# Kernel optimization log

Hardware: AMD Instinct MI355X
Metric: run time of the kernel (lower is better)

## Reference

```python
import jax, jax.numpy as jnp
import numpy as np

B, L, H, C, K, S = 32, 512, 336, 321, 8, 8   # batch, seq_len, pred_len, channels, leaders, states
FREQ = H // 2 + 1                            # 169
G = 2 * K + 1                                # filter groups
TEMP = 1.0
EPS = 1e-5


def setup_inputs() -> dict:
    key = jax.random.key(0)
    ks = jax.random.split(key, 12)
    x = jax.random.normal(ks[0], (B, L, C), jnp.float32)
    leader_ids = jax.random.randint(ks[1], (B, C, K), 0, C)
    shift = jax.random.randint(ks[2], (B, C, K), 0, L)
    r = jax.random.normal(ks[3], (B, C, K), jnp.float32)
    # backbone linear: seq_len -> pred_len
    Wb = jax.random.normal(ks[4], (H, L), jnp.float32) * float(1.0 / np.sqrt(L))
    bb = jnp.zeros((H,), jnp.float32)
    # factory classifier: (L + K) features -> state_num logits
    Wc = jax.random.normal(ks[5], (S, L + K), jnp.float32) * float(1.0 / np.sqrt(L + K))
    bc = jnp.zeros((S,), jnp.float32)
    # state prototype filters (complex, stored as re/im): [S, 2K+1, FREQ]
    states_re = jax.random.normal(ks[6], (S, G, FREQ), jnp.float32) * float(1.0 / np.sqrt(S))
    states_im = jax.random.normal(ks[7], (S, G, FREQ), jnp.float32) * float(1.0 / np.sqrt(S))
    # complex mix layer: 3*FREQ -> FREQ
    Wm_re = jax.random.normal(ks[8], (FREQ, 3 * FREQ), jnp.float32) * float(1.0 / np.sqrt(3 * FREQ))
    Wm_im = jax.random.normal(ks[9], (FREQ, 3 * FREQ), jnp.float32) * float(1.0 / np.sqrt(3 * FREQ))
    bm_re = jnp.zeros((FREQ,), jnp.float32)
    bm_im = jnp.zeros((FREQ,), jnp.float32)
    return dict(x=x, r=r, Wb=Wb, bb=bb, Wc=Wc, bc=bc,
                states_re=states_re, states_im=states_im,
                Wm_re=Wm_re, Wm_im=Wm_im, bm_re=bm_re, bm_im=bm_im,
                leader_ids=leader_ids, shift=shift)


def reference(x, r, Wb, bb, Wc, bc, states_re, states_im, Wm_re, Wm_im, bm_re, bm_im, leader_ids, shift):
    xc = jnp.transpose(x, (0, 2, 1))                      # [B,C,L]
    mu = xc.mean(-1, keepdims=True)
    norm = jnp.sqrt(xc.var(-1, keepdims=True) + EPS)
    xn = (xc - mu) / norm                                 # instance_norm
    y_hat = jnp.einsum('bcl,hl->bch', xn, Wb) + bb        # backbone [B,C,H]

    # --- shifted_leader_seq (torch.no_grad) ---
    full = jax.lax.stop_gradient(jnp.concatenate([xn, y_hat], -1))      # [B,C,L+H]
    lead_full = full[jnp.arange(B)[:, None, None], leader_ids]          # [B,C,K,L+H]
    t_idx = (L - shift)[..., None] + jnp.arange(H)                      # [B,C,K,H]
    seq_shifted = jnp.take_along_axis(lead_full, t_idx, axis=-1)        # [B,C,K,H]
    r = jax.lax.stop_gradient(r)

    # softmax leader weights with leading constant-one slot
    ones = jnp.ones((B, C, 1), xn.dtype)
    r_soft = jax.nn.softmax(jnp.concatenate([ones, jnp.abs(r)], -1) / TEMP, axis=-1)  # [B,C,K+1]

    # --- factory: state-mixed complex filters ---
    feat = jnp.concatenate([xn, r_soft[..., 1:]], -1)                   # [B,C,L+K]
    p = jax.nn.softmax(jnp.einsum('bcf,sf->bcs', feat, Wc) + bc, axis=-1)
    states = states_re + 1j * states_im                                 # [S,G,FREQ]
    filters = jnp.einsum('bcs,sgf->bcgf', p, states)                    # [B,C,2K+1,FREQ]

    # --- FFT filter multiply-sum + inverse FFT mix ---
    y_hat_f = jnp.fft.rfft(y_hat)                                       # [B,C,FREQ]
    seq_shifted_f = jnp.fft.rfft(seq_shifted) * filters[:, :, :K]       # [B,C,K,FREQ]
    seq_diff_f = (seq_shifted_f - y_hat_f[:, :, None]) * filters[:, :, K:-1]
    yh_f = y_hat_f * filters[:, :, -1]
    z = jnp.concatenate([seq_shifted_f.sum(2), seq_diff_f.sum(2), yh_f], -1)  # [B,C,3*FREQ]
    Wm = Wm_re + 1j * Wm_im
    mixed = jnp.einsum('bcf,gf->bcg', z, Wm) + (bm_re + 1j * bm_im)     # [B,C,FREQ]
    y_hat = y_hat + jnp.fft.irfft(mixed, n=H)

    y = y_hat * norm + mu
    return jnp.transpose(y, (0, 2, 1))                                  # [B,H,C]
```

## Files before the change

### kernel.cpp

```cpp
#include <hip/hip_runtime.h>
#include <math.h>

#define B_ 32
#define L_ 512
#define H_ 336
#define C_ 321
#define K_ 8
#define S_ 8
#define FREQ_ 169
#define G_ 17
#define LHB_ 848
#define F_FEAT 520
#define EPS_ 1e-5f
#define BCN_ (B_ * C_)
#define DZB_ 7

#ifndef M_PIf
#define M_PIf 3.14159265358979323846f
#endif

typedef __attribute__((ext_vector_type(8))) short short8v;
typedef __attribute__((ext_vector_type(4))) float f32x4;

__device__ __forceinline__ unsigned short f2bf(float x) {
    unsigned u = __builtin_bit_cast(unsigned, x);
    u += 0x7FFFu + ((u >> 16) & 1u);
    return (unsigned short)(u >> 16);
}
__device__ __forceinline__ float bf2f(unsigned short h) {
    return __builtin_bit_cast(float, (unsigned)h << 16);
}

__global__ __launch_bounds__(256) void k_prepA(const float* __restrict__ Wb,
                                               const float* __restrict__ st_re,
                                               const float* __restrict__ st_im,
                                               unsigned short* __restrict__ Tdft,
                                               float* __restrict__ ctb,
                                               float* __restrict__ stb,
                                               unsigned short* __restrict__ Wbsw,
                                               float4* __restrict__ stf4,
                                               float2* __restrict__ stg3) {
    int bid = blockIdx.x, tid = threadIdx.x;
    if (bid < 61) {
        int orig = bid * 4 + (tid >> 6);
        if (orig < 11 * 22) {
            int lane = tid & 63;
            int kc = orig / 22, nt = orig % 22;
            int n = nt * 16 + (lane & 15);
            int kb = kc * 32 + (lane >> 4) * 8;
            int f = n >> 1;
            unsigned short* dst = Tdft + (size_t)orig * 512 + lane * 8;
            for (int i = 0; i < 8; ++i) {
                int k = kb + i;
                float val = 0.f;
                if (k < H_ && n < 2 * FREQ_) {
                    int m = (k * f) % H_;
                    float s, c;
                    sincosf((float)m * (2.0f * M_PIf / (float)H_), &s, &c);
                    val = (n & 1) ? -s : c;
                }
                dst[i] = f2bf(val);
            }
        }
    } else if (bid < 283) {
        int idx = (bid - 61) * 256 + tid;
        if (idx < FREQ_ * H_) {
            int g = idx / H_, h = idx % H_;
            int m = (g * h) % H_;
            float s, c;
            sincosf((float)m * (2.0f * M_PIf / (float)H_), &s, &c);
            float wgt = ((g == 0 || g == FREQ_ - 1) ? 1.0f : 2.0f) * (1.0f / (float)H_);
            ctb[idx] = wgt * c;
            stb[idx] = -wgt * s;
        }
    } else if (bid < 367) {
        int orig = (bid - 283) * 4 + (tid >> 6);
        if (orig < 16 * 21) {
            int lane = tid & 63;
            int kc = orig / 21, nt = orig % 21;
            int n = nt * 16 + (lane & 15);
            int kb = kc * 32 + (lane >> 4) * 8;
            unsigned short* dst = Wbsw + (size_t)orig * 512 + lane * 8;
            for (int i = 0; i < 8; ++i) {
                int k = kb + i;
                dst[i] = f2bf(Wb[(size_t)n * L_ + k]);
            }
        }
    } else {
        int idx = (bid - 367) * 256 + tid;
        if (idx < 64 * FREQ_) {
            int row = idx / FREQ_, f = idx % FREQ_;
            int k = row >> 3, s = row & 7;
            size_t b1 = (size_t)s * (G_ * FREQ_) + (size_t)k * FREQ_ + f;
            size_t b2 = (size_t)s * (G_ * FREQ_) + (size_t)(8 + k) * FREQ_ + f;
            stf4[idx] = make_float4(st_re[b1], st_im[b1], st_re[b2], st_im[b2]);
        }
        if (idx < 8 * FREQ_) {
            int s = idx / FREQ_, f = idx % FREQ_;
            size_t b3 = (size_t)s * (G_ * FREQ_) + (size_t)16 * FREQ_ + f;
            stg3[idx] = make_float2(st_re[b3], st_im[b3]);
        }
    }
}

__global__ __launch_bounds__(256) void k_prepB(const float* __restrict__ Wm_re,
                                               const float* __restrict__ Wm_im,
                                               const float* __restrict__ bm_re,
                                               const float* __restrict__ bm_im,
                                               const float* __restrict__ ctb,
                                               const float* __restrict__ stb,
                                               unsigned short* __restrict__ T,
                                               float* __restrict__ bvec) {
    int bid = blockIdx.x, tid = threadIdx.x;
    if (bid < 672) {
        int t = bid * 256 + tid;
        if (t >= 512 * H_) return;
        int k = t / H_, h = t - k * H_;
        float s1 = 0.f, s2 = 0.f;
        if (k < 3 * FREQ_) {
            #pragma unroll 4
            for (int g = 0; g < FREQ_; ++g) {
                float ct = ctb[g * H_ + h];
                float st = stb[g * H_ + h];
                float wr = Wm_re[(size_t)g * (3 * FREQ_) + k];
                float wi = Wm_im[(size_t)g * (3 * FREQ_) + k];
                s1 += wr * ct + wi * st;
                s2 += wr * st - wi * ct;
            }
        }
        int nt = h >> 4, nr = h & 15;
        {
            int kc = k >> 5, kr = k & 31;
            int lane = ((kr >> 3) << 4) | nr;
            T[((size_t)(kc * 21 + nt)) * 512 + lane * 8 + (k & 7)] = f2bf(s1);
        }
        {
            int kk = k + 512;
            int kc = kk >> 5, kr = kk & 31;
            int lane = ((kr >> 3) << 4) | nr;
            T[((size_t)(kc * 21 + nt)) * 512 + lane * 8 + (kk & 7)] = f2bf(s2);
        }
    } else {
        int h = (bid - 672) * 256 + tid;
        if (h >= H_) return;
        float acc = 0.f;
        for (int g = 0; g < FREQ_; ++g)
            acc += bm_re[g] * ctb[g * H_ + h] + bm_im[g] * stb[g * H_ + h];
        bvec[h] = acc;
    }
}

__global__ __launch_bounds__(256) void k_stats_part(const float* __restrict__ x,
                                                    float2* __restrict__ part) {
    __shared__ float red_s[4][64], red_q[4][64];
    int tid = threadIdx.x, w = tid >> 6, lane = tid & 63;
    int b = blockIdx.y, c0 = blockIdx.x * 64, l0 = blockIdx.z * 64;
    int c = c0 + lane;
    bool valid = (c < C_);
    const float* xb = x + ((size_t)b * L_) * C_;
    float s = 0.f, q = 0.f;
    for (int li = w; li < 64; li += 4) {
        float v = valid ? xb[(size_t)(l0 + li) * C_ + c] : 0.f;
        s += v; q += v * v;
    }
    red_s[w][lane] = s; red_q[w][lane] = q;
    __syncthreads();
    if (w == 0) {
        float S = red_s[0][lane] + red_s[1][lane] + red_s[2][lane] + red_s[3][lane];
        float Q = red_q[0][lane] + red_q[1][lane] + red_q[2][lane] + red_q[3][lane];
        part[(size_t)(((b * 6 + blockIdx.x) * 8) + blockIdx.z) * 64 + lane] = make_float2(S, Q);
    }
}

__global__ __launch_bounds__(256) void k_stats_fin(const float2* __restrict__ part,
                                                   float* __restrict__ muv,
                                                   float* __restrict__ nrm) {
    int t = blockIdx.x * 256 + threadIdx.x;
    int b = t / 384, rem = t % 384;
    int ct = rem / 64, cl = rem % 64;
    int c = ct * 64 + cl;
    if (b >= B_ || c >= C_) return;
    float S = 0.f, Q = 0.f;
    #pragma unroll
    for (int ls = 0; ls < 8; ++ls) {
        float2 p = part[(size_t)(((b * 6 + ct) * 8) + ls) * 64 + cl];
        S += p.x; Q += p.y;
    }
    float mu = S / (float)L_;
    float var = Q / (float)L_ - mu * mu;
    float n = sqrtf(var + EPS_);
    muv[(size_t)b * C_ + c] = mu;
    nrm[(size_t)b * C_ + c] = n;
}

__global__ __launch_bounds__(256) void k_norm(const float* __restrict__ x,
                                              const float* __restrict__ muv,
                                              const float* __restrict__ nrm,
                                              unsigned short* __restrict__ fullbf) {
    __shared__ float tl[64][65];
    int tid = threadIdx.x, w = tid >> 6, lane = tid & 63;
    int b = blockIdx.y, c0 = blockIdx.x * 64, l0 = blockIdx.z * 64;
    int c = c0 + lane;
    bool valid = (c < C_);
    const float* xb = x + ((size_t)b * L_) * C_;
    float mu = valid ? muv[(size_t)b * C_ + c] : 0.f;
    float inv = valid ? (1.0f / nrm[(size_t)b * C_ + c]) : 0.f;
    for (int li = w; li < 64; li += 4) {
        float v = valid ? xb[(size_t)(l0 + li) * C_ + c] : 0.f;
        tl[li][lane] = (v - mu) * inv;
    }
    __syncthreads();
    for (int cr = w; cr < 64; cr += 4) {
        int cc = c0 + cr;
        if (cc < C_ && lane < 32) {
            size_t bc = (size_t)b * C_ + cc;
            unsigned pk = (unsigned)f2bf(tl[2 * lane][cr]) |
                          ((unsigned)f2bf(tl[2 * lane + 1][cr]) << 16);
            ((unsigned*)fullbf)[(bc * LHB_ + l0) / 2 + lane] = pk;
        }
    }
}

__global__ __launch_bounds__(256) void k_yhat(const unsigned short* __restrict__ fullbf_r,
                                              const unsigned short* __restrict__ Wbsw,
                                              const float* __restrict__ bb,
                                              unsigned short* __restrict__ fullbf_w) {
    int bc0 = blockIdx.x * 32;
    int half = blockIdx.y;
    int tid = threadIdx.x, w = tid >> 6, lane = tid & 63;
    const int NTB0[5] = {0, 3, 6, 9, 11};
    const int NTB1[5] = {11, 14, 17, 19, 21};
    int nt0 = half ? NTB1[w] : NTB0[w];
    int ntn = (half ? NTB1[w + 1] : NTB0[w + 1]) - nt0;
    int r15 = lane & 15, kg = lane >> 4;
    f32x4 acc[2][3];
    #pragma unroll
    for (int mf = 0; mf < 2; ++mf)
        #pragma unroll
        for (int j = 0; j < 3; ++j) acc[mf][j] = (f32x4){0.f, 0.f, 0.f, 0.f};
    for (int kc = 0; kc < 16; ++kc) {
        short8v a[2];
        #pragma unroll
        for (int mf = 0; mf < 2; ++mf)
            a[mf] = *(const short8v*)(fullbf_r + ((size_t)(bc0 + mf * 16 + r15) * LHB_ + kc * 32 + kg * 8));
        #pragma unroll
        for (int j = 0; j < 3; ++j) {
            if (j >= ntn) continue;
            short8v bfr = *(const short8v*)(Wbsw + ((size_t)(kc * 21 + nt0 + j) * 512 + lane * 8));
            #pragma unroll
            for (int mf = 0; mf < 2; ++mf)
                acc[mf][j] = __builtin_amdgcn_mfma_f32_16x16x32_bf16(a[mf], bfr, acc[mf][j], 0, 0, 0);
        }
    }
    #pragma unroll
    for (int mf = 0; mf < 2; ++mf)
        #pragma unroll
        for (int j = 0; j < 3; ++j) {
            if (j >= ntn) continue;
            int n_ = (nt0 + j) * 16 + r15;
            #pragma unroll
            for (int reg = 0; reg < 4; ++reg) {
                int bc = bc0 + mf * 16 + kg * 4 + reg;
                fullbf_w[(size_t)bc * LHB_ + L_ + n_] = f2bf(acc[mf][j][reg] + bb[n_]);
            }
        }
}

__global__ __launch_bounds__(256) void k_p2(const unsigned short* __restrict__ fullbf,
                                            const float* __restrict__ r,
                                            const float* __restrict__ Wc,
                                            const float* __restrict__ bcv,
                                            float* __restrict__ p_out) {
    __shared__ float WcS[8 * F_FEAT];
    __shared__ float rsS[16][8];
    __shared__ float bcS[8];
    int tid = threadIdx.x, w = tid >> 6, lane = tid & 63;
    int bc0 = blockIdx.x * 16;
    for (int i = tid; i < 8 * F_FEAT; i += 256) WcS[i] = Wc[i];
    if (tid < 8) bcS[tid] = bcv[tid];
    if (tid < 16) {
        int bc = bc0 + tid;
        const float* rr = r + (size_t)bc * K_;
        float a[8]; float m = 1.0f;
        #pragma unroll
        for (int k = 0; k < 8; ++k) { a[k] = fabsf(rr[k]); m = fmaxf(m, a[k]); }
        float Z = expf(1.0f - m);
        float e[8];
        #pragma unroll
        for (int k = 0; k < 8; ++k) { e[k] = expf(a[k] - m); Z += e[k]; }
        float inv = 1.0f / Z;
        #pragma unroll
        for (int k = 0; k < 8; ++k) rsS[tid][k] = e[k] * inv;
    }
    __syncthreads();

    for (int i = 0; i < 4; ++i) {
        int bcl = w * 4 + i;
        int bc = bc0 + bcl;
        const unsigned* xrow = (const unsigned*)(fullbf + (size_t)bc * LHB_);
        float acc[8] = {0.f, 0.f, 0.f, 0.f, 0.f, 0.f, 0.f, 0.f};
        #pragma unroll
        for (int t = 0; t < 4; ++t) {
            int j = lane + t * 64;
            unsigned v = xrow[j];
            float x0 = bf2f((unsigned short)(v & 0xffff));
            float x1 = bf2f((unsigned short)(v >> 16));
            #pragma unroll
            for (int s = 0; s < 8; ++s)
                acc[s] += x0 * WcS[s * F_FEAT + 2 * j] + x1 * WcS[s * F_FEAT + 2 * j + 1];
        }
        if (lane < 8) {
            float xf = rsS[bcl][lane];
            #pragma unroll
            for (int s = 0; s < 8; ++s) acc[s] += xf * WcS[s * F_FEAT + L_ + lane];
        }
        #pragma unroll
        for (int s = 0; s < 8; ++s) {
            #pragma unroll
            for (int off = 32; off > 0; off >>= 1) acc[s] += __shfl_down(acc[s], off);
        }
        if (lane == 0) {
            float m = -1e30f;
            #pragma unroll
            for (int s = 0; s < 8; ++s) { acc[s] += bcS[s]; m = fmaxf(m, acc[s]); }
            float Z = 0.f; float e[8];
            #pragma unroll
            for (int s = 0; s < 8; ++s) { e[s] = expf(acc[s] - m); Z += e[s]; }
            float inv = 1.0f / Z;
            #pragma unroll
            for (int s = 0; s < 8; ++s) p_out[(size_t)bc * 8 + s] = e[s] * inv;
        }
    }
}

__global__ __launch_bounds__(512) void k_dftz2(const unsigned short* __restrict__ fullbf,
                                               const int* __restrict__ leader,
                                               const int* __restrict__ shiftp,
                                               const unsigned short* __restrict__ Tsw,
                                               const float* __restrict__ pbuf,
                                               const float4* __restrict__ stf4,
                                               const float2* __restrict__ stg3,
                                               unsigned short* __restrict__ zbf) {
    __shared__ unsigned short A[64 * 360];
    __shared__ float psL[DZB_][8];
    int tid = threadIdx.x, w = tid >> 6, lane = tid & 63;
    int bc0 = blockIdx.x * DZB_;
    unsigned* A32 = (unsigned*)A;
    for (int i = tid; i < 64 * 180; i += 512) A32[i] = 0;
    if (tid < DZB_ * 8) {
        int bcl = tid >> 3, s = tid & 7;
        int bc = bc0 + bcl;
        psL[bcl][s] = (bc < BCN_) ? pbuf[(size_t)bc * 8 + s] : 0.f;
    }
    if (tid >= 64 && tid < 64 + DZB_ * 10) {
        int t = tid - 64;
        int bcl = t / 10, o = t - bcl * 10;
        int bc = bc0 + bcl;
        if (bc < BCN_) {
            unsigned short* zrow = zbf + (size_t)bc * 1024;
            if (o < 5) zrow[507 + o] = 0;
            else       zrow[1019 + (o - 5)] = 0;
        }
    }
    __syncthreads();

    #pragma unroll
    for (int i = 0; i < 8; ++i) {
        int rr = w * 8 + i;
        if (rr >= 63) break;
        int bcl = rr / 9, k = rr - bcl * 9;
        int bc = bc0 + bcl;
        if (bc < BCN_) {
            int b = bc / C_;
            const unsigned short* src;
            if (k < 8) {
                int lead = leader[(size_t)bc * K_ + k];
                int sh = shiftp[(size_t)bc * K_ + k];
                src = fullbf + ((size_t)b * C_ + lead) * LHB_ + (L_ - sh);
            } else {
                src = fullbf + (size_t)bc * LHB_ + L_;
            }
            unsigned short* dst = A + rr * 360;
            #pragma unroll
            for (int t = 0; t < 6; ++t) {
                int j = lane + t * 64;
                if (j < H_) dst[j] = src[j];
            }
        }
    }
    __syncthreads();

    const int NTB[9] = {0, 3, 6, 9, 11, 14, 17, 20, 22};
    int nt0 = NTB[w], ntn = NTB[w + 1] - nt0;
    int r15 = lane & 15, kg = lane >> 4;
    f32x4 acc[4][3];
    #pragma unroll
    for (int mf = 0; mf < 4; ++mf)
        #pragma unroll
        for (int j = 0; j < 3; ++j) acc[mf][j] = (f32x4){0.f, 0.f, 0.f, 0.f};
    for (int kc = 0; kc < 11; ++kc) {
        short8v a[4];
        #pragma unroll
        for (int mf = 0; mf < 4; ++mf)
            a[mf] = *(const short8v*)(A + (size_t)(mf * 16 + r15) * 360 + kc * 32 + kg * 8);
        #pragma unroll
        for (int j = 0; j < 3; ++j) {
            if (j >= ntn) continue;
            short8v bfr = *(const short8v*)(Tsw + ((size_t)(kc * 22 + nt0 + j) * 512 + lane * 8));
            #pragma unroll
            for (int mf = 0; mf < 4; ++mf)
                acc[mf][j] = __builtin_amdgcn_mfma_f32_16x16x32_bf16(a[mf], bfr, acc[mf][j], 0, 0, 0);
        }
    }
    __syncthreads();

    #pragma unroll
    for (int mf = 0; mf < 4; ++mf)
        #pragma unroll
        for (int j = 0; j < 3; ++j) {
            if (j >= ntn) continue;
            int col = (nt0 + j) * 16 + r15;
            #pragma unroll
            for (int reg = 0; reg < 4; ++reg) {
                int row = mf * 16 + kg * 4 + reg;
                A[row * 360 + col] = f2bf(acc[mf][j][reg]);
            }
        }
    __syncthreads();

    if (tid < 507) {
        int g = tid / 169;
        int f = tid - g * 169;
        int bclo = (g == 0) ? 0 : (g == 1) ? 3 : 5;
        int nb   = (g == 0) ? 3 : 2;
        float z1r[3], z1i[3], z2r[3], z2i[3], Yr[3], Yi[3];
        #pragma unroll
        for (int bl = 0; bl < 3; ++bl) {
            z1r[bl] = z1i[bl] = z2r[bl] = z2i[bl] = 0.f;
            unsigned v = (bl < nb) ? A32[((bclo + bl) * 9 + 8) * 180 + f] : 0u;
            Yr[bl] = bf2f((unsigned short)(v & 0xffff));
            Yi[bl] = bf2f((unsigned short)(v >> 16));
        }
        for (int k = 0; k < 8; ++k) {
            float4 stv[8];
            #pragma unroll
            for (int s = 0; s < 8; ++s) stv[s] = stf4[(size_t)(k * 8 + s) * FREQ_ + f];
            #pragma unroll
            for (int bl = 0; bl < 3; ++bl) {
                if (bl >= nb) continue;
                int bcl = bclo + bl;
                float f1r = 0.f, f1i = 0.f, f2r = 0.f, f2i = 0.f;
                #pragma unroll
                for (int s = 0; s < 8; ++s) {
                    float p = psL[bcl][s];
                    f1r += p * stv[s].x; f1i += p * stv[s].y;
                    f2r += p * stv[s].z; f2i += p * stv[s].w;
                }
                unsigned v = A32[(bcl * 9 + k) * 180 + f];
                float Xr = bf2f((unsigned short)(v & 0xffff));
                float Xi = bf2f((unsigned short)(v >> 16));
                float ar = Xr * f1r - Xi * f1i;
                float ai = Xr * f1i + Xi * f1r;
                z1r[bl] += ar; z1i[bl] += ai;
                float dr = ar - Yr[bl], di = ai - Yi[bl];
                z2r[bl] += dr * f2r - di * f2i;
                z2i[bl] += dr * f2i + di * f2r;
            }
        }
        #pragma unroll
        for (int bl = 0; bl < 3; ++bl) {
            if (bl >= nb) continue;
            int bcl = bclo + bl;
            int bc = bc0 + bcl;
            if (bc >= BCN_) continue;
            float f3r = 0.f, f3i = 0.f;
            #pragma unroll
            for (int s = 0; s < 8; ++s) {
                float2 v3 = stg3[(size_t)s * FREQ_ + f];
                float p = psL[bcl][s];
                f3r += p * v3.x; f3i += p * v3.y;
            }
            unsigned short* zrow = zbf + (size_t)bc * 1024;
            zrow[f]       = f2bf(z1r[bl]);  zrow[512 + f]       = f2bf(z1i[bl]);
            zrow[169 + f] = f2bf(z2r[bl]);  zrow[512 + 169 + f] = f2bf(z2i[bl]);
            zrow[338 + f] = f2bf(Yr[bl] * f3r - Yi[bl] * f3i);
            zrow[512 + 338 + f] = f2bf(Yr[bl] * f3i + Yi[bl] * f3r);
        }
    }
}

__global__ __launch_bounds__(256) void k_mixf2(const unsigned short* __restrict__ zbf,
                                               const unsigned short* __restrict__ WTsw,
                                               const float* __restrict__ bvec,
                                               const unsigned short* __restrict__ fullbf,
                                               const float* __restrict__ muv,
                                               const float* __restrict__ nrm,
                                               float* __restrict__ out) {
    __shared__ float ytile[32][177];
    int bc0 = blockIdx.x * 32;
    int half = blockIdx.y;
    int tid = threadIdx.x, w = tid >> 6, lane = tid & 63;
    const int NTB0[5] = {0, 3, 6, 9, 11};
    const int NTB1[5] = {11, 14, 17, 19, 21};
    int nt0 = half ? NTB1[w] : NTB0[w];
    int ntn = (half ? NTB1[w + 1] : NTB0[w + 1]) - nt0;
    int h0 = half ? 176 : 0;
    int hn = half ? 160 : 176;
    int r15 = lane & 15, kg = lane >> 4;
    f32x4 acc[2][3];
    #pragma unroll
    for (int mf = 0; mf < 2; ++mf)
        #pragma unroll
        for (int j = 0; j < 3; ++j) acc[mf][j] = (f32x4){0.f, 0.f, 0.f, 0.f};
    for (int kc = 0; kc < 32; ++kc) {
        short8v a[2];
        #pragma unroll
        for (int mf = 0; mf < 2; ++mf)
            a[mf] = *(const short8v*)(zbf + ((size_t)(bc0 + mf * 16 + r15) * 1024 + kc * 32 + kg * 8));
        #pragma unroll
        for (int j = 0; j < 3; ++j) {
            if (j >= ntn) continue;
            short8v bfr = *(const short8v*)(WTsw + ((size_t)(kc * 21 + nt0 + j) * 512 + lane * 8));
            #pragma unroll
            for (int mf = 0; mf < 2; ++mf)
                acc[mf][j] = __builtin_amdgcn_mfma_f32_16x16x32_bf16(a[mf], bfr, acc[mf][j], 0, 0, 0);
        }
    }
    #pragma unroll
    for (int mf = 0; mf < 2; ++mf)
        #pragma unroll
        for (int j = 0; j < 3; ++j) {
            if (j >= ntn) continue;
            int h = (nt0 + j) * 16 + r15;
            float bv = bvec[h];
            #pragma unroll
            for (int reg = 0; reg < 4; ++reg) {
                int bcl = mf * 16 + kg * 4 + reg;
                int bc = bc0 + bcl;
                float yh = bf2f(fullbf[(size_t)bc * LHB_ + L_ + h]);
                float y = (yh + acc[mf][j][reg] + bv) * nrm[bc] + muv[bc];
                ytile[bcl][h - h0] = y;
            }
        }
    __syncthreads();
    for (int idx = tid; idx < 32 * hn; idx += 256) {
        int bcl = idx & 31, hrel = idx >> 5;
        int bc = bc0 + bcl;
        int b = bc / C_, c = bc - b * C_;
        out[((size_t)b * H_ + h0 + hrel) * C_ + c] = ytile[bcl][hrel];
    }
}

extern "C" void kernel_launch(void* const* d_in, const int* in_sizes, int n_in,
                              void* d_out, int out_size, void* d_ws, size_t ws_size,
                              hipStream_t stream) {
    const float* x     = (const float*)d_in[0];
    const float* r     = (const float*)d_in[1];
    const float* Wb    = (const float*)d_in[2];
    const float* bb    = (const float*)d_in[3];
    const float* Wc    = (const float*)d_in[4];
    const float* bcv   = (const float*)d_in[5];
    const float* st_re = (const float*)d_in[6];
    const float* st_im = (const float*)d_in[7];
    const float* Wm_re = (const float*)d_in[8];
    const float* Wm_im = (const float*)d_in[9];
    const float* bm_re = (const float*)d_in[10];
    const float* bm_im = (const float*)d_in[11];
    const int* leader  = (const int*)d_in[12];
    const int* shiftp  = (const int*)d_in[13];
    float* out = (float*)d_out;

    char* w = (char*)d_ws;
    auto carve = [&](size_t bytes) {
        char* p = w;
        w += (bytes + 255) & ~(size_t)255;
        return (void*)p;
    };
    unsigned short* Tdft = (unsigned short*)carve((size_t)11 * 22 * 512 * 2);
    unsigned short* WTsw = (unsigned short*)carve((size_t)32 * 21 * 512 * 2);
    unsigned short* Wbsw = (unsigned short*)carve((size_t)16 * 21 * 512 * 2);
    float*          ctb  = (float*)carve((size_t)FREQ_ * H_ * 4);
    float*          stb  = (float*)carve((size_t)FREQ_ * H_ * 4);
    float*          bvec = (float*)carve((size_t)H_ * 4);
    float4*         stf4 = (float4*)carve((size_t)64 * FREQ_ * 16);
    float2*         stg3 = (float2*)carve((size_t)8 * FREQ_ * 8);
    float2*         part = (float2*)carve((size_t)B_ * 6 * 8 * 64 * 8);
    unsigned short* fullbf = (unsigned short*)carve((size_t)BCN_ * LHB_ * 2);
    float*          muv  = (float*)carve((size_t)BCN_ * 4);
    float*          nrm  = (float*)carve((size_t)BCN_ * 4);
    float*          pbuf = (float*)carve((size_t)BCN_ * 8 * 4);
    unsigned short* zbf  = (unsigned short*)carve((size_t)BCN_ * 1024 * 2);

    hipLaunchKernelGGL(k_prepA, dim3(410), dim3(256), 0, stream,
                       Wb, st_re, st_im, Tdft, ctb, stb, Wbsw, stf4, stg3);
    hipLaunchKernelGGL(k_prepB, dim3(674), dim3(256), 0, stream,
                       Wm_re, Wm_im, bm_re, bm_im, ctb, stb, WTsw, bvec);
    hipLaunchKernelGGL(k_stats_part, dim3(6, 32, 8), dim3(256), 0, stream, x, part);
    hipLaunchKernelGGL(k_stats_fin, dim3(48), dim3(256), 0, stream, part, muv, nrm);
    hipLaunchKernelGGL(k_norm, dim3(6, 32, 8), dim3(256), 0, stream, x, muv, nrm, fullbf);
    hipLaunchKernelGGL(k_yhat, dim3(BCN_ / 32, 2), dim3(256), 0, stream, fullbf, Wbsw, bb, fullbf);
    hipLaunchKernelGGL(k_p2, dim3(BCN_ / 16), dim3(256), 0, stream, fullbf, r, Wc, bcv, pbuf);
    hipLaunchKernelGGL(k_dftz2, dim3((BCN_ + DZB_ - 1) / DZB_), dim3(512), 0, stream,
                       fullbf, leader, shiftp, Tdft, pbuf, stf4, stg3, zbf);
    hipLaunchKernelGGL(k_mixf2, dim3(BCN_ / 32, 2), dim3(256), 0, stream,
                       zbf, WTsw, bvec, fullbf, muv, nrm, out);
}
```

Baseline: 226.2 us.

## Fuse instance-norm stats and normalize into one kernel; co-launch yhat and classifier

Replaces the three-kernel stats/finalize/normalize chain with one kernel per (batch, 32-channel tile) that computes mean/variance in shared memory and then writes normalized bf16 rows. It also merges the backbone MFMA GEMM and the factory classifier into one launch partitioned by block index. This removes launches, the partial-sum buffer round trip and the serialization between y_hat and the classifier, at the cost of fewer, larger blocks for the norm (352 blocks) and x being read twice inside one kernel.

```diff
diff --git a/kernel.cpp b/kernel.cpp
--- a/kernel.cpp
+++ b/kernel.cpp
@@ -150,185 +150,176 @@
     }
 }
 
-__global__ __launch_bounds__(256) void k_stats_part(const float* __restrict__ x,
-                                                    float2* __restrict__ part) {
-    __shared__ float red_s[4][64], red_q[4][64];
-    int tid = threadIdx.x, w = tid >> 6, lane = tid & 63;
-    int b = blockIdx.y, c0 = blockIdx.x * 64, l0 = blockIdx.z * 64;
-    int c = c0 + lane;
+__global__ __launch_bounds__(512) void k_ln3(const float* __restrict__ x,
+                                             unsigned short* __restrict__ fullbf,
+                                             float* __restrict__ muv,
+                                             float* __restrict__ nrm) {
+    __shared__ float red_s[16][32], red_q[16][32];
+    __shared__ float sMu[32], sInv[32];
+    __shared__ float tl[64][33];
+    int tid = threadIdx.x;
+    int c_l = tid & 31, lg = tid >> 5;
+    int b = blockIdx.y, c0 = blockIdx.x * 32;
+    int c = c0 + c_l;
     bool valid = (c < C_);
-    const float* xb = x + ((size_t)b * L_) * C_;
+    const float* xb = x + (size_t)b * L_ * C_;
+
     float s = 0.f, q = 0.f;
-    for (int li = w; li < 64; li += 4) {
-        float v = valid ? xb[(size_t)(l0 + li) * C_ + c] : 0.f;
+    #pragma unroll 8
+    for (int i = 0; i < 32; ++i) {
+        int l = lg * 32 + i;
+        float v = valid ? xb[(size_t)l * C_ + c] : 0.f;
         s += v; q += v * v;
     }
-    red_s[w][lane] = s; red_q[w][lane] = q;
-    __syncthreads();
-    if (w == 0) {
-        float S = red_s[0][lane] + red_s[1][lane] + red_s[2][lane] + red_s[3][lane];
-        float Q = red_q[0][lane] + red_q[1][lane] + red_q[2][lane] + red_q[3][lane];
-        part[(size_t)(((b * 6 + blockIdx.x) * 8) + blockIdx.z) * 64 + lane] = make_float2(S, Q);
-    }
-}
-
-__global__ __launch_bounds__(256) void k_stats_fin(const float2* __restrict__ part,
-                                                   float* __restrict__ muv,
-                                                   float* __restrict__ nrm) {
-    int t = blockIdx.x * 256 + threadIdx.x;
-    int b = t / 384, rem = t % 384;
-    int ct = rem / 64, cl = rem % 64;
-    int c = ct * 64 + cl;
-    if (b >= B_ || c >= C_) return;
-    float S = 0.f, Q = 0.f;
-    #pragma unroll
-    for (int ls = 0; ls < 8; ++ls) {
-        float2 p = part[(size_t)(((b * 6 + ct) * 8) + ls) * 64 + cl];
-        S += p.x; Q += p.y;
-    }
-    float mu = S / (float)L_;
-    float var = Q / (float)L_ - mu * mu;
-    float n = sqrtf(var + EPS_);
-    muv[(size_t)b * C_ + c] = mu;
-    nrm[(size_t)b * C_ + c] = n;
-}
-
-__global__ __launch_bounds__(256) void k_norm(const float* __restrict__ x,
-                                              const float* __restrict__ muv,
-                                              const float* __restrict__ nrm,
-                                              unsigned short* __restrict__ fullbf) {
-    __shared__ float tl[64][65];
-    int tid = threadIdx.x, w = tid >> 6, lane = tid & 63;
-    int b = blockIdx.y, c0 = blockIdx.x * 64, l0 = blockIdx.z * 64;
-    int c = c0 + lane;
-    bool valid = (c < C_);
-    const float* xb = x + ((size_t)b * L_) * C_;
-    float mu = valid ? muv[(size_t)b * C_ + c] : 0.f;
-    float inv = valid ? (1.0f / nrm[(size_t)b * C_ + c]) : 0.f;
-    for (int li = w; li < 64; li += 4) {
-        float v = valid ? xb[(size_t)(l0 + li) * C_ + c] : 0.f;
-        tl[li][lane] = (v - mu) * inv;
-    }
-    __syncthreads();
-    for (int cr = w; cr < 64; cr += 4) {
-        int cc = c0 + cr;
-        if (cc < C_ && lane < 32) {
-            size_t bc = (size_t)b * C_ + cc;
-            unsigned pk = (unsigned)f2bf(tl[2 * lane][cr]) |
-                          ((unsigned)f2bf(tl[2 * lane + 1][cr]) << 16);
-            ((unsigned*)fullbf)[(bc * LHB_ + l0) / 2 + lane] = pk;
-        }
-    }
-}
-
-__global__ __launch_bounds__(256) void k_yhat(const unsigned short* __restrict__ fullbf_r,
-                                              const unsigned short* __restrict__ Wbsw,
-                                              const float* __restrict__ bb,
-                                              unsigned short* __restrict__ fullbf_w) {
-    int bc0 = blockIdx.x * 32;
-    int half = blockIdx.y;
-    int tid = threadIdx.x, w = tid >> 6, lane = tid & 63;
-    const int NTB0[5] = {0, 3, 6, 9, 11};
-    const int NTB1[5] = {11, 14, 17, 19, 21};
-    int nt0 = half ? NTB1[w] : NTB0[w];
-    int ntn = (half ? NTB1[w + 1] : NTB0[w + 1]) - nt0;
-    int r15 = lane & 15, kg = lane >> 4;
-    f32x4 acc[2][3];
-    #pragma unroll
-    for (int mf = 0; mf < 2; ++mf)
-        #pragma unroll
-        for (int j = 0; j < 3; ++j) acc[mf][j] = (f32x4){0.f, 0.f, 0.f, 0.f};
-    for (int kc = 0; kc < 16; ++kc) {
-        short8v a[2];
-        #pragma unroll
-        for (int mf = 0; mf < 2; ++mf)
-            a[mf] = *(const short8v*)(fullbf_r + ((size_t)(bc0 + mf * 16 + r15) * LHB_ + kc * 32 + kg * 8));
-        #pragma unroll
-        for (int j = 0; j < 3; ++j) {
-            if (j >= ntn) continue;
-            short8v bfr = *(const short8v*)(Wbsw + ((size_t)(kc * 21 + nt0 + j) * 512 + lane * 8));
-            #pragma unroll
-            for (int mf = 0; mf < 2; ++mf)
-                acc[mf][j] = __builtin_amdgcn_mfma_f32_16x16x32_bf16(a[mf], bfr, acc[mf][j], 0, 0, 0);
-        }
-    }
-    #pragma unroll
-    for (int mf = 0; mf < 2; ++mf)
-        #pragma unroll
-        for (int j = 0; j < 3; ++j) {
-            if (j >= ntn) continue;
-            int n_ = (nt0 + j) * 16 + r15;
-            #pragma unroll
-            for (int reg = 0; reg < 4; ++reg) {
-                int bc = bc0 + mf * 16 + kg * 4 + reg;
-                fullbf_w[(size_t)bc * LHB_ + L_ + n_] = f2bf(acc[mf][j][reg] + bb[n_]);
-            }
-        }
-}
-
-__global__ __launch_bounds__(256) void k_p2(const unsigned short* __restrict__ fullbf,
+    red_s[lg][c_l] = s; red_q[lg][c_l] = q;
+    __syncthreads();
+    if (tid < 32) {
+        float S = 0.f, Q = 0.f;
+        #pragma unroll
+        for (int g = 0; g < 16; ++g) { S += red_s[g][tid]; Q += red_q[g][tid]; }
+        float mu = S / (float)L_;
+        float var = Q / (float)L_ - mu * mu;
+        float n = sqrtf(var + EPS_);
+        sMu[tid] = mu; sInv[tid] = 1.0f / n;
+        if (c0 + tid < C_) {
+            muv[(size_t)b * C_ + c0 + tid] = mu;
+            nrm[(size_t)b * C_ + c0 + tid] = n;
+        }
+    }
+    __syncthreads();
+    float mu = sMu[c_l], inv = sInv[c_l];
+
+    for (int l0 = 0; l0 < L_; l0 += 64) {
+        for (int li = lg; li < 64; li += 16) {
+            float v = valid ? xb[(size_t)(l0 + li) * C_ + c] : 0.f;
+            tl[li][c_l] = (v - mu) * inv;
+        }
+        __syncthreads();
+        #pragma unroll
+        for (int t = 0; t < 2; ++t) {
+            int idx = tid + t * 512;
+            int cr = idx >> 5, j = idx & 31;
+            int cc = c0 + cr;
+            if (cc < C_) {
+                size_t bc = (size_t)b * C_ + cc;
+                unsigned pk = (unsigned)f2bf(tl[2 * j][cr]) |
+                              ((unsigned)f2bf(tl[2 * j + 1][cr]) << 16);
+                ((unsigned*)fullbf)[(bc * LHB_ + l0) / 2 + j] = pk;
+            }
+        }
+        __syncthreads();
+    }
+}
+
+__global__ __launch_bounds__(256) void k_hp(const unsigned short* __restrict__ fullbf,
+                                            const unsigned short* __restrict__ Wbsw,
+                                            const float* __restrict__ bb,
                                             const float* __restrict__ r,
                                             const float* __restrict__ Wc,
                                             const float* __restrict__ bcv,
+                                            unsigned short* __restrict__ fullbf_w,
                                             float* __restrict__ p_out) {
     __shared__ float WcS[8 * F_FEAT];
     __shared__ float rsS[16][8];
     __shared__ float bcS[8];
+    int bid = blockIdx.x;
     int tid = threadIdx.x, w = tid >> 6, lane = tid & 63;
-    int bc0 = blockIdx.x * 16;
-    for (int i = tid; i < 8 * F_FEAT; i += 256) WcS[i] = Wc[i];
-    if (tid < 8) bcS[tid] = bcv[tid];
-    if (tid < 16) {
-        int bc = bc0 + tid;
-        const float* rr = r + (size_t)bc * K_;
-        float a[8]; float m = 1.0f;
-        #pragma unroll
-        for (int k = 0; k < 8; ++k) { a[k] = fabsf(rr[k]); m = fmaxf(m, a[k]); }
-        float Z = expf(1.0f - m);
-        float e[8];
-        #pragma unroll
-        for (int k = 0; k < 8; ++k) { e[k] = expf(a[k] - m); Z += e[k]; }
-        float inv = 1.0f / Z;
-        #pragma unroll
-        for (int k = 0; k < 8; ++k) rsS[tid][k] = e[k] * inv;
-    }
-    __syncthreads();
-
-    for (int i = 0; i < 4; ++i) {
-        int bcl = w * 4 + i;
-        int bc = bc0 + bcl;
-        const unsigned* xrow = (const unsigned*)(fullbf + (size_t)bc * LHB_);
-        float acc[8] = {0.f, 0.f, 0.f, 0.f, 0.f, 0.f, 0.f, 0.f};
-        #pragma unroll
-        for (int t = 0; t < 4; ++t) {
-            int j = lane + t * 64;
-            unsigned v = xrow[j];
-            float x0 = bf2f((unsigned short)(v & 0xffff));
-            float x1 = bf2f((unsigned short)(v >> 16));
-            #pragma unroll
-            for (int s = 0; s < 8; ++s)
-                acc[s] += x0 * WcS[s * F_FEAT + 2 * j] + x1 * WcS[s * F_FEAT + 2 * j + 1];
-        }
-        if (lane < 8) {
-            float xf = rsS[bcl][lane];
-            #pragma unroll
-            for (int s = 0; s < 8; ++s) acc[s] += xf * WcS[s * F_FEAT + L_ + lane];
-        }
-        #pragma unroll
-        for (int s = 0; s < 8; ++s) {
-            #pragma unroll
-            for (int off = 32; off > 0; off >>= 1) acc[s] += __shfl_down(acc[s], off);
-        }
-        if (lane == 0) {
-            float m = -1e30f;
-            #pragma unroll
-            for (int s = 0; s < 8; ++s) { acc[s] += bcS[s]; m = fmaxf(m, acc[s]); }
-            float Z = 0.f; float e[8];
-            #pragma unroll
-            for (int s = 0; s < 8; ++s) { e[s] = expf(acc[s] - m); Z += e[s]; }
+
+    if (bid < 642) {
+        int bc0 = (bid >> 1) * 32;
+        int half = bid & 1;
+        const int NTB0[5] = {0, 3, 6, 9, 11};
+        const int NTB1[5] = {11, 14, 17, 19, 21};
+        int nt0 = half ? NTB1[w] : NTB0[w];
+        int ntn = (half ? NTB1[w + 1] : NTB0[w + 1]) - nt0;
+        int r15 = lane & 15, kg = lane >> 4;
+        f32x4 acc[2][3];
+        #pragma unroll
+        for (int mf = 0; mf < 2; ++mf)
+            #pragma unroll
+            for (int j = 0; j < 3; ++j) acc[mf][j] = (f32x4){0.f, 0.f, 0.f, 0.f};
+        for (int kc = 0; kc < 16; ++kc) {
+            short8v a[2];
+            #pragma unroll
+            for (int mf = 0; mf < 2; ++mf)
+                a[mf] = *(const short8v*)(fullbf + ((size_t)(bc0 + mf * 16 + r15) * LHB_ + kc * 32 + kg * 8));
+            #pragma unroll
+            for (int j = 0; j < 3; ++j) {
+                if (j >= ntn) continue;
+                short8v bfr = *(const short8v*)(Wbsw + ((size_t)(kc * 21 + nt0 + j) * 512 + lane * 8));
+                #pragma unroll
+                for (int mf = 0; mf < 2; ++mf)
+                    acc[mf][j] = __builtin_amdgcn_mfma_f32_16x16x32_bf16(a[mf], bfr, acc[mf][j], 0, 0, 0);
+            }
+        }
+        #pragma unroll
+        for (int mf = 0; mf < 2; ++mf)
+            #pragma unroll
+            for (int j = 0; j < 3; ++j) {
+                if (j >= ntn) continue;
+                int n_ = (nt0 + j) * 16 + r15;
+                #pragma unroll
+                for (int reg = 0; reg < 4; ++reg) {
+                    int bc = bc0 + mf * 16 + kg * 4 + reg;
+                    fullbf_w[(size_t)bc * LHB_ + L_ + n_] = f2bf(acc[mf][j][reg] + bb[n_]);
+                }
+            }
+    } else {
+        int bc0 = (bid - 642) * 16;
+        for (int i = tid; i < 8 * F_FEAT; i += 256) WcS[i] = Wc[i];
+        if (tid < 8) bcS[tid] = bcv[tid];
+        if (tid < 16) {
+            int bc = bc0 + tid;
+            const float* rr = r + (size_t)bc * K_;
+            float a[8]; float m = 1.0f;
+            #pragma unroll
+            for (int k = 0; k < 8; ++k) { a[k] = fabsf(rr[k]); m = fmaxf(m, a[k]); }
+            float Z = expf(1.0f - m);
+            float e[8];
+            #pragma unroll
+            for (int k = 0; k < 8; ++k) { e[k] = expf(a[k] - m); Z += e[k]; }
             float inv = 1.0f / Z;
             #pragma unroll
-            for (int s = 0; s < 8; ++s) p_out[(size_t)bc * 8 + s] = e[s] * inv;
+            for (int k = 0; k < 8; ++k) rsS[tid][k] = e[k] * inv;
+        }
+        __syncthreads();
+
+        for (int i = 0; i < 4; ++i) {
+            int bcl = w * 4 + i;
+            int bc = bc0 + bcl;
+            const unsigned* xrow = (const unsigned*)(fullbf + (size_t)bc * LHB_);
+            float acc[8] = {0.f, 0.f, 0.f, 0.f, 0.f, 0.f, 0.f, 0.f};
+            #pragma unroll
+            for (int t = 0; t < 4; ++t) {
+                int j = lane + t * 64;
+                unsigned v = xrow[j];
+                float x0 = bf2f((unsigned short)(v & 0xffff));
+                float x1 = bf2f((unsigned short)(v >> 16));
+                #pragma unroll
+                for (int s = 0; s < 8; ++s)
+                    acc[s] += x0 * WcS[s * F_FEAT + 2 * j] + x1 * WcS[s * F_FEAT + 2 * j + 1];
+            }
+            if (lane < 8) {
+                float xf = rsS[bcl][lane];
+                #pragma unroll
+                for (int s = 0; s < 8; ++s) acc[s] += xf * WcS[s * F_FEAT + L_ + lane];
+            }
+            #pragma unroll
+            for (int s = 0; s < 8; ++s) {
+                #pragma unroll
+                for (int off = 32; off > 0; off >>= 1) acc[s] += __shfl_down(acc[s], off);
+            }
+            if (lane == 0) {
+                float m = -1e30f;
+                #pragma unroll
+                for (int s = 0; s < 8; ++s) { acc[s] += bcS[s]; m = fmaxf(m, acc[s]); }
+                float Z = 0.f; float e[8];
+                #pragma unroll
+                for (int s = 0; s < 8; ++s) { e[s] = expf(acc[s] - m); Z += e[s]; }
+                float inv = 1.0f / Z;
+                #pragma unroll
+                for (int s = 0; s < 8; ++s) p_out[(size_t)bc * 8 + s] = e[s] * inv;
+            }
         }
     }
 }
@@ -584,7 +575,6 @@
     float*          bvec = (float*)carve((size_t)H_ * 4);
     float4*         stf4 = (float4*)carve((size_t)64 * FREQ_ * 16);
     float2*         stg3 = (float2*)carve((size_t)8 * FREQ_ * 8);
-    float2*         part = (float2*)carve((size_t)B_ * 6 * 8 * 64 * 8);
     unsigned short* fullbf = (unsigned short*)carve((size_t)BCN_ * LHB_ * 2);
     float*          muv  = (float*)carve((size_t)BCN_ * 4);
     float*          nrm  = (float*)carve((size_t)BCN_ * 4);
@@ -595,11 +585,9 @@
                        Wb, st_re, st_im, Tdft, ctb, stb, Wbsw, stf4, stg3);
     hipLaunchKernelGGL(k_prepB, dim3(674), dim3(256), 0, stream,
                        Wm_re, Wm_im, bm_re, bm_im, ctb, stb, WTsw, bvec);
-    hipLaunchKernelGGL(k_stats_part, dim3(6, 32, 8), dim3(256), 0, stream, x, part);
-    hipLaunchKernelGGL(k_stats_fin, dim3(48), dim3(256), 0, stream, part, muv, nrm);
-    hipLaunchKernelGGL(k_norm, dim3(6, 32, 8), dim3(256), 0, stream, x, muv, nrm, fullbf);
-    hipLaunchKernelGGL(k_yhat, dim3(BCN_ / 32, 2), dim3(256), 0, stream, fullbf, Wbsw, bb, fullbf);
-    hipLaunchKernelGGL(k_p2, dim3(BCN_ / 16), dim3(256), 0, stream, fullbf, r, Wc, bcv, pbuf);
+    hipLaunchKernelGGL(k_ln3, dim3(11, 32), dim3(512), 0, stream, x, fullbf, muv, nrm);
+    hipLaunchKernelGGL(k_hp, dim3(642 + 642), dim3(256), 0, stream,
+                       fullbf, Wbsw, bb, r, Wc, bcv, fullbf, pbuf);
     hipLaunchKernelGGL(k_dftz2, dim3((BCN_ + DZB_ - 1) / DZB_), dim3(512), 0, stream,
                        fullbf, leader, shiftp, Tdft, pbuf, stf4, stg3, zbf);
     hipLaunchKernelGGL(k_mixf2, dim3(BCN_ / 32, 2), dim3(256), 0, stream,
```

Result: no change. 222.0 us, median of 3 (-1.9%).
